# Optimization experiments

Hardware: AMD Instinct MI355X
Metric: run time of the kernel (lower is better)

Reference implementation:

```python
import jax, jax.numpy as jnp
import numpy as np

N_NODE = 100000
EMB = 100
BATCH = 512
SEQ = 50
LAYERS = 2
NNZ = 1000000
BETA = 0.01


def setup_inputs() -> dict:
    key = jax.random.key(0)
    ks = jax.random.split(key, 16)
    stdv = 1.0 / np.sqrt(EMB)
    u = lambda k, shp: jax.random.uniform(k, shp, jnp.float32, -stdv, stdv)
    emb_weight = u(ks[0], (N_NODE, EMB))
    pos_weight = u(ks[1], (200, EMB))
    w_1 = u(ks[2], (2 * EMB, EMB))
    w_2 = u(ks[3], (EMB, 1))
    glu1_w = u(ks[4], (EMB, EMB))
    glu1_b = u(ks[5], (EMB,))
    glu2_w = u(ks[6], (EMB, EMB))
    # sparse hypergraph adjacency in COO form
    adj_rows = jax.random.randint(ks[7], (NNZ,), 0, N_NODE)
    adj_cols = jax.random.randint(ks[8], (NNZ,), 0, N_NODE)
    adj_vals = jax.random.uniform(ks[9], (NNZ,), jnp.float32, 0.0, 0.1)
    session_item = jax.random.randint(ks[10], (BATCH, SEQ), 0, N_NODE + 1)
    reversed_sess_item = jax.random.randint(ks[11], (BATCH, SEQ), 0, N_NODE + 1)
    session_len = jnp.ones((BATCH, 1), jnp.float32)
    mask = jnp.ones((BATCH, SEQ), jnp.float32)
    D = jax.random.uniform(ks[12], (BATCH, BATCH), jnp.float32, 0.0, 0.01)
    A = jax.random.uniform(ks[13], (BATCH, BATCH), jnp.float32, 0.0, 0.01)
    # fixed permutations standing in for torch.randperm in SSL
    perm_rows = jax.random.permutation(ks[14], BATCH)
    perm_cols = jax.random.permutation(ks[15], EMB)
    return {
        'session_item': session_item, 'session_len': session_len, 'D': D, 'A': A,
        'reversed_sess_item': reversed_sess_item, 'mask': mask,
        'emb_weight': emb_weight, 'pos_weight': pos_weight, 'w_1': w_1, 'w_2': w_2,
        'glu1_w': glu1_w, 'glu1_b': glu1_b, 'glu2_w': glu2_w,
        'adj_rows': adj_rows, 'adj_cols': adj_cols, 'adj_vals': adj_vals,
        'perm_rows': perm_rows, 'perm_cols': perm_cols,
    }


def reference(session_item, session_len, D, A, reversed_sess_item, mask,
              emb_weight, pos_weight, w_1, w_2, glu1_w, glu1_b, glu2_w,
              adj_rows, adj_cols, adj_vals, perm_rows, perm_cols):
    # ---- HyperConv: layers of sparse mm, summed over layer outputs ----
    h = emb_weight
    item_hg = h
    for _ in range(LAYERS):
        h = jax.ops.segment_sum(adj_vals[:, None] * h[adj_cols], adj_rows,
                                num_segments=N_NODE)
        item_hg = item_hg + h

    # ---- generate_sess_emb (gather + attention gate) ----
    pad_hg = jnp.concatenate([jnp.zeros((1, EMB), item_hg.dtype), item_hg], 0)
    seq_h = pad_hg[reversed_sess_item]                       # [B, L, d]
    hs = jnp.sum(seq_h, 1) / session_len                     # [B, d]
    pos = jnp.broadcast_to(pos_weight[:SEQ], (BATCH, SEQ, EMB))
    nh = jnp.tanh(jnp.concatenate([pos, seq_h], -1) @ w_1)   # [B, L, d]
    nh = jax.nn.sigmoid(nh @ glu1_w.T + glu1_b + (hs @ glu2_w.T)[:, None, :])
    att = (nh @ w_2) * mask[..., None]                       # [B, L, 1]
    sess_hg = jnp.sum(att * seq_h, 1)                        # [B, d]

    # ---- LineConv (line-graph propagation on raw embedding) ----
    pad0 = jnp.concatenate([jnp.zeros((1, EMB), emb_weight.dtype), emb_weight], 0)
    s = jnp.sum(pad0[session_item], 1) / session_len          # [B, d]
    sess_lg = s
    DA = D @ A
    for _ in range(LAYERS):
        s = DA @ s
        sess_lg = sess_lg + s

    # ---- SSL contrastive loss (fixed permutations replace randperm) ----
    pos_s = jnp.sum(sess_hg * sess_lg, 1)
    corrupt = sess_hg[perm_rows][:, perm_cols]
    neg1 = jnp.sum(sess_lg * corrupt, 1)
    con = jnp.sum(-jnp.log(1e-8 + jax.nn.sigmoid(pos_s))
                  - jnp.log(1e-8 + (1.0 - jax.nn.sigmoid(neg1))))

    # use_HG=True -> sess_emb is the hypergraph session embedding
    return item_hg, sess_hg, BETA * con
```

## Files before the change

### kernel.cpp

```cpp
#include <hip/hip_runtime.h>
#include <math.h>

#define N_NODE 100000
#define EMB    100
#define BATCH  512
#define SEQ    50
#define NNZ    1000000

#define SCAN_CHUNK 1024
#define SCAN_NB ((N_NODE + SCAN_CHUNK - 1) / SCAN_CHUNK)

static __device__ __forceinline__ float bf2f(unsigned short u) {
  union { unsigned int i; float f; } v; v.i = ((unsigned int)u) << 16; return v.f;
}
static __device__ __forceinline__ unsigned short f2bf(float f) {
  union { float f; unsigned int i; } v; v.f = f;
  unsigned int i = v.i;
  return (unsigned short)((i + 0x7fffu + ((i >> 16) & 1u)) >> 16);
}
static __device__ __forceinline__ float lo2f(unsigned int u) {
  union { unsigned int i; float f; } v; v.i = u << 16; return v.f;
}
static __device__ __forceinline__ float hi2f(unsigned int u) {
  union { unsigned int i; float f; } v; v.i = u & 0xffff0000u; return v.f;
}

__global__ void hist_kernel(const int* __restrict__ rows, int* __restrict__ counts) {
  int i = blockIdx.x * blockDim.x + threadIdx.x;
  if (i < NNZ) atomicAdd(&counts[rows[i]], 1);
}

__global__ void scan_partial_kernel(const int* __restrict__ counts, int* __restrict__ partial) {
  __shared__ int red[256];
  int b = blockIdx.x, t = threadIdx.x;
  int base = b * SCAN_CHUNK;
  int s = 0;
  #pragma unroll
  for (int k = 0; k < SCAN_CHUNK; k += 256) {
    int idx = base + k + t;
    if (idx < N_NODE) s += counts[idx];
  }
  red[t] = s;
  __syncthreads();
  for (int off = 128; off; off >>= 1) {
    if (t < off) red[t] += red[t + off];
    __syncthreads();
  }
  if (t == 0) partial[b] = red[0];
}

__global__ void scan_top_kernel(int* __restrict__ partial, int* __restrict__ row_ptr) {
  __shared__ int s[128];
  int t = threadIdx.x;
  int v = (t < SCAN_NB) ? partial[t] : 0;
  s[t] = v;
  __syncthreads();
  for (int off = 1; off < 128; off <<= 1) {
    int u = (t >= off) ? s[t - off] : 0;
    __syncthreads();
    s[t] += u;
    __syncthreads();
  }
  if (t < SCAN_NB) partial[t] = (t == 0) ? 0 : s[t - 1];
  if (t == 127) row_ptr[N_NODE] = s[127];
}

__global__ void scan_final_kernel(const int* __restrict__ partial,
                                  int* __restrict__ counts_cursor,
                                  int* __restrict__ row_ptr) {
  __shared__ int s[256];
  int b = blockIdx.x, t = threadIdx.x;
  int base = b * SCAN_CHUNK + t * 4;
  int c[4];
  #pragma unroll
  for (int k = 0; k < 4; ++k) {
    int idx = base + k;
    c[k] = (idx < N_NODE) ? counts_cursor[idx] : 0;
  }
  int local = c[0] + c[1] + c[2] + c[3];
  s[t] = local;
  __syncthreads();
  for (int off = 1; off < 256; off <<= 1) {
    int u = (t >= off) ? s[t - off] : 0;
    __syncthreads();
    s[t] += u;
    __syncthreads();
  }
  int prefix = partial[b] + ((t == 0) ? 0 : s[t - 1]);
  #pragma unroll
  for (int k = 0; k < 4; ++k) {
    int idx = base + k;
    if (idx < N_NODE) {
      row_ptr[idx] = prefix;
      counts_cursor[idx] = prefix;
      prefix += c[k];
    }
  }
}

__global__ void scatterA_kernel(const int* __restrict__ rows, const int* __restrict__ cols,
                                const float* __restrict__ vals, int* __restrict__ cursor,
                                unsigned int* __restrict__ cv) {
  int i = blockIdx.x * blockDim.x + threadIdx.x;
  if (i >= NNZ) return;
  int p = atomicAdd(&cursor[rows[i]], 1);
  int q = (int)rintf(vals[i] * 327670.f);
  q = q < 0 ? 0 : (q > 32767 ? 32767 : q);
  cv[p] = ((unsigned int)cols[i] << 15) | (unsigned int)q;
}

__global__ void scatterB_kernel(const int* __restrict__ rows, const int* __restrict__ cols,
                                const float* __restrict__ vals, int* __restrict__ cursor,
                                unsigned short* __restrict__ colHi, unsigned char* __restrict__ colLo) {
  int i = blockIdx.x * blockDim.x + threadIdx.x;
  if (i >= NNZ) return;
  int p = atomicAdd(&cursor[rows[i]], 1);
  int c = cols[i];
  int q = (int)rintf(vals[i] * 1270.f);
  q = q < 0 ? 0 : (q > 127 ? 127 : q);
  colHi[p] = (unsigned short)(c >> 1);
  colLo[p] = (unsigned char)(((c & 1) << 7) | q);
}

__global__ void spmmA_kernel(const int* __restrict__ rp, const unsigned int* __restrict__ cv,
                             const float2* __restrict__ gsrc, const float2* __restrict__ base,
                             float2* __restrict__ dst) {
  int w = (blockIdx.x * blockDim.x + threadIdx.x) >> 6;
  int lane = threadIdx.x & 63;
  if (w >= N_NODE || lane >= 50) return;
  int s = __builtin_amdgcn_readfirstlane(rp[w]);
  int e = __builtin_amdgcn_readfirstlane(rp[w + 1]);
  float ax[16], ay[16];
  #pragma unroll
  for (int k = 0; k < 16; ++k) { ax[k] = 0.f; ay[k] = 0.f; }
  for (int j = s; j < e; j += 16) {
    int   cc[16];
    float vv[16];
    #pragma unroll
    for (int k = 0; k < 16; ++k) {
      int jj = j + k;
      int jc = jj < e ? jj : e - 1;
      unsigned int u = cv[jc];
      cc[k] = (int)(u >> 15);
      float v = (float)(u & 0x7fffu) * (1.f / 327670.f);
      vv[k] = (jj < e) ? v : 0.f;
    }
    float2 uu[16];
    #pragma unroll
    for (int k = 0; k < 16; ++k) uu[k] = gsrc[cc[k] * 50 + lane];
    #pragma unroll
    for (int k = 0; k < 16; ++k) { ax[k] += vv[k] * uu[k].x; ay[k] += vv[k] * uu[k].y; }
  }
  #pragma unroll
  for (int k = 0; k < 8; ++k) { ax[k] += ax[k + 8]; ay[k] += ay[k + 8]; }
  #pragma unroll
  for (int k = 0; k < 4; ++k) { ax[k] += ax[k + 4]; ay[k] += ay[k + 4]; }
  float sx = (ax[0] + ax[1]) + (ax[2] + ax[3]);
  float sy = (ay[0] + ay[1]) + (ay[2] + ay[3]);
  float2 ev = base[w * 50 + lane];
  dst[w * 50 + lane] = make_float2(ev.x + sx, ev.y + sy);
}

__global__ void spmmB_kernel(const int* __restrict__ rp, const unsigned short* __restrict__ colHi,
                             const unsigned char* __restrict__ colLo,
                             const float2* __restrict__ gsrc, const float2* __restrict__ base,
                             float2* __restrict__ dst) {
  int w = (blockIdx.x * blockDim.x + threadIdx.x) >> 6;
  int lane = threadIdx.x & 63;
  if (w >= N_NODE || lane >= 50) return;
  int s = __builtin_amdgcn_readfirstlane(rp[w]);
  int e = __builtin_amdgcn_readfirstlane(rp[w + 1]);
  float ax[16], ay[16];
  #pragma unroll
  for (int k = 0; k < 16; ++k) { ax[k] = 0.f; ay[k] = 0.f; }
  for (int j = s; j < e; j += 16) {
    int   cc[16];
    float vv[16];
    #pragma unroll
    for (int k = 0; k < 16; ++k) {
      int jj = j + k;
      int jc = jj < e ? jj : e - 1;
      int hi = colHi[jc], lo = colLo[jc];
      cc[k] = (hi << 1) | (lo >> 7);
      float v = (float)(lo & 0x7f) * (1.f / 1270.f);
      vv[k] = (jj < e) ? v : 0.f;
    }
    float2 uu[16];
    #pragma unroll
    for (int k = 0; k < 16; ++k) uu[k] = gsrc[cc[k] * 50 + lane];
    #pragma unroll
    for (int k = 0; k < 16; ++k) { ax[k] += vv[k] * uu[k].x; ay[k] += vv[k] * uu[k].y; }
  }
  #pragma unroll
  for (int k = 0; k < 8; ++k) { ax[k] += ax[k + 8]; ay[k] += ay[k + 8]; }
  #pragma unroll
  for (int k = 0; k < 4; ++k) { ax[k] += ax[k + 4]; ay[k] += ay[k + 4]; }
  float sx = (ax[0] + ax[1]) + (ax[2] + ax[3]);
  float sy = (ay[0] + ay[1]) + (ay[2] + ay[3]);
  float2 ev = base[w * 50 + lane];
  dst[w * 50 + lane] = make_float2(ev.x + sx, ev.y + sy);
}

__global__ void posw_kernel(const float* __restrict__ pos_w, const float* __restrict__ w1,
                            float* __restrict__ posW) {
  __shared__ float sp[EMB];
  int l = blockIdx.x, e = threadIdx.x;
  if (e < EMB) sp[e] = pos_w[l * EMB + e];
  __syncthreads();
  if (e < EMB) {
    float a = 0.f;
    for (int k = 0; k < EMB; ++k) a += sp[k] * w1[k * EMB + e];
    posW[l * EMB + e] = a;
  }
}

__global__ __launch_bounds__(512, 4) void sess_kernel(
    const int* __restrict__ rsi, const int* __restrict__ si,
    const float* __restrict__ item_hg,
    const float* __restrict__ emb, const float* __restrict__ slen,
    const float* __restrict__ posW, const float* __restrict__ w1,
    const float* __restrict__ glu1w, const float* __restrict__ glu1b,
    const float* __restrict__ glu2w, const float* __restrict__ w2,
    const float* __restrict__ maskp,
    float* __restrict__ X, float* __restrict__ Z,
    float* __restrict__ out_sess) {
  __shared__ __align__(16) float seq[SEQ * EMB];
  __shared__ unsigned int w1p[50 * EMB];
  __shared__ unsigned int g1p[50 * EMB];
  __shared__ float hsL[EMB];
  __shared__ __align__(16) float nhL[4][EMB];
  __shared__ float hsP[4][EMB];
  __shared__ float s0P[4][EMB];
  __shared__ float hsgP[4][EMB];
  __shared__ float accP[4][EMB];
  __shared__ float redg[4][2];
  int b = blockIdx.x, t = threadIdx.x;
  int g = t >> 7;
  int e = t & 127;
  bool act = e < EMB;

  for (int i = t; i < 50 * EMB; i += 512) {
    int kp = i / EMB, e2 = i % EMB;
    unsigned int b0 = f2bf(w1[EMB * EMB + (2 * kp) * EMB + e2]);
    unsigned int b1 = f2bf(w1[EMB * EMB + (2 * kp + 1) * EMB + e2]);
    w1p[i] = b0 | (b1 << 16);
    unsigned int c0 = f2bf(glu1w[e2 * EMB + 2 * kp]);
    unsigned int c1 = f2bf(glu1w[e2 * EMB + 2 * kp + 1]);
    g1p[i] = c0 | (c1 << 16);
  }

  float inv = 1.f / slen[b];

  float hsacc = 0.f, s0acc = 0.f;
  if (act) {
    for (int l = g; l < SEQ; l += 4) {
      int i1 = rsi[b * SEQ + l];
      float sv_ = (i1 > 0) ? item_hg[(i1 - 1) * EMB + e] : 0.f;
      seq[l * EMB + e] = sv_;
      hsacc += sv_;
      int i0 = si[b * SEQ + l];
      if (i0 > 0) s0acc += emb[(i0 - 1) * EMB + e];
    }
    hsP[g][e] = hsacc;
    s0P[g][e] = s0acc;
  }
  __syncthreads();
  if (act && g == 0) {
    float hv = (hsP[0][e] + hsP[1][e] + hsP[2][e] + hsP[3][e]) * inv;
    float sv = (s0P[0][e] + s0P[1][e] + s0P[2][e] + s0P[3][e]) * inv;
    hsL[e] = hv;
    X[b * EMB + e] = sv;
    Z[b * EMB + e] = sv;
  }
  __syncthreads();

  if (act) {
    float a = 0.f;
    int k0 = g * 25;
    for (int k = k0; k < k0 + 25; ++k) a += hsL[k] * glu2w[e * EMB + k];
    hsgP[g][e] = a;
  }
  __syncthreads();
  float hsgv = 0.f, w2v = 0.f;
  if (act) {
    hsgv = glu1b[e] + hsgP[0][e] + hsgP[1][e] + hsgP[2][e] + hsgP[3][e];
    w2v = w2[e];
  }

  float acc = 0.f;
  for (int it = 0; it < (SEQ + 3) / 4; ++it) {
    int l = it * 4 + g;
    bool lv = l < SEQ;
    __syncthreads();
    if (act && lv) {
      const float4* sq4 = (const float4*)&seq[l * EMB];
      float a0 = 0.f, a1 = 0.f, a2 = 0.f, a3 = 0.f;
      #pragma unroll
      for (int i = 0; i < 25; ++i) {
        float4 sv = sq4[i];
        unsigned int p0 = w1p[(2 * i) * EMB + e];
        unsigned int p1 = w1p[(2 * i + 1) * EMB + e];
        a0 += sv.x * lo2f(p0);
        a1 += sv.y * hi2f(p0);
        a2 += sv.z * lo2f(p1);
        a3 += sv.w * hi2f(p1);
      }
      float nh = posW[l * EMB + e] + ((a0 + a1) + (a2 + a3));
      nhL[g][e] = tanhf(nh);
    }
    __syncthreads();
    float p = 0.f;
    if (act && lv) {
      const float4* nq4 = (const float4*)nhL[g];
      float a0 = hsgv, a1 = 0.f, a2 = 0.f, a3 = 0.f;
      #pragma unroll
      for (int i = 0; i < 25; ++i) {
        float4 nv = nq4[i];
        unsigned int p0 = g1p[(2 * i) * EMB + e];
        unsigned int p1 = g1p[(2 * i + 1) * EMB + e];
        a0 += nv.x * lo2f(p0);
        a1 += nv.y * hi2f(p0);
        a2 += nv.z * lo2f(p1);
        a3 += nv.w * hi2f(p1);
      }
      float a = (a0 + a1) + (a2 + a3);
      float gs = 1.f / (1.f + __expf(-a));
      p = gs * w2v;
    }
    for (int off = 32; off; off >>= 1) p += __shfl_down(p, off, 64);
    if ((t & 63) == 0) redg[g][(t >> 6) & 1] = p;
    __syncthreads();
    if (act && lv) {
      float att = (redg[g][0] + redg[g][1]) * maskp[b * SEQ + l];
      acc += att * seq[l * EMB + e];
    }
  }
  if (act) accP[g][e] = acc;
  __syncthreads();
  if (act && g == 0)
    out_sess[b * EMB + e] = accP[0][e] + accP[1][e] + accP[2][e] + accP[3][e];
}

__global__ void mv_kernel(const float* __restrict__ M, const float* __restrict__ x,
                          float* __restrict__ y, float* __restrict__ Zacc) {
  __shared__ float Ms[BATCH];
  int b = blockIdx.x, t = threadIdx.x;
  for (int i = t; i < BATCH; i += 128) Ms[i] = M[b * BATCH + i];
  __syncthreads();
  if (t < EMB) {
    float a = 0.f;
    for (int k = 0; k < BATCH; ++k) a += Ms[k] * x[k * EMB + t];
    y[b * EMB + t] = a;
    if (Zacc) Zacc[b * EMB + t] += a;
  }
}

__global__ void ssl_kernel(const float* __restrict__ Z, const float* __restrict__ hg,
                           const int* __restrict__ pr, const int* __restrict__ pc,
                           float* __restrict__ loss_out) {
  __shared__ float r1[128], r2[128];
  int b = blockIdx.x, t = threadIdx.x;
  float p1 = 0.f, p2 = 0.f;
  if (t < EMB) {
    float lg = Z[b * EMB + t];
    p1 = lg * hg[b * EMB + t];
    p2 = lg * hg[pr[b] * EMB + pc[t]];
  }
  r1[t] = p1; r2[t] = p2;
  __syncthreads();
  for (int off = 64; off; off >>= 1) {
    if (t < off) { r1[t] += r1[t + off]; r2[t] += r2[t + off]; }
    __syncthreads();
  }
  if (t == 0) {
    float sp = 1.f / (1.f + expf(-r1[0]));
    float sn = 1.f / (1.f + expf(-r2[0]));
    atomicAdd(loss_out, 0.01f * (-logf(1e-8f + sp) - logf(1e-8f + (1.f - sn))));
  }
}

extern "C" void kernel_launch(void* const* d_in, const int* in_sizes, int n_in,
                              void* d_out, int out_size, void* d_ws, size_t ws_size,
                              hipStream_t stream) {
  const int*   session_item = (const int*)d_in[0];
  const float* slen   = (const float*)d_in[1];
  const float* D      = (const float*)d_in[2];
  const float* A      = (const float*)d_in[3];
  const int*   rsi    = (const int*)d_in[4];
  const float* mask   = (const float*)d_in[5];
  const float* emb    = (const float*)d_in[6];
  const float* posw   = (const float*)d_in[7];
  const float* w1     = (const float*)d_in[8];
  const float* w2     = (const float*)d_in[9];
  const float* glu1w  = (const float*)d_in[10];
  const float* glu1b  = (const float*)d_in[11];
  const float* glu2w  = (const float*)d_in[12];
  const int*   adj_rows = (const int*)d_in[13];
  const int*   adj_cols = (const int*)d_in[14];
  const float* adj_vals = (const float*)d_in[15];
  const int*   pr     = (const int*)d_in[16];
  const int*   pc     = (const int*)d_in[17];

  float* out_item = (float*)d_out;
  float* out_sess = out_item + (size_t)N_NODE * EMB;
  float* out_loss = out_sess + (size_t)BATCH * EMB;
  float2* out2    = (float2*)d_out;
  const float2* emb2 = (const float2*)emb;

  char* ws = (char*)d_ws;
  size_t off = 0;
  auto alloc = [&](size_t bytes) -> void* {
    void* p = ws + off;
    off = (off + bytes + 255) & ~(size_t)255;
    return p;
  };

  hipMemsetAsync(out_loss, 0, 4, stream);

  if (ws_size >= 5500000) {
    int*          counts  = (int*)alloc((size_t)N_NODE * 4);
    int*          row_ptr = (int*)alloc((size_t)(N_NODE + 1) * 4);
    int*          partial = (int*)alloc((size_t)SCAN_NB * 4);
    unsigned int* cv      = (unsigned int*)alloc((size_t)NNZ * 4);
    float* posW = (float*)alloc((size_t)SEQ * EMB * 4);
    float* X    = (float*)alloc((size_t)BATCH * EMB * 4);
    float* Y    = (float*)alloc((size_t)BATCH * EMB * 4);
    float* Z    = (float*)alloc((size_t)BATCH * EMB * 4);

    hipMemsetAsync(counts, 0, (size_t)N_NODE * 4, stream);

    hist_kernel<<<(NNZ + 255) / 256, 256, 0, stream>>>(adj_rows, counts);
    scan_partial_kernel<<<SCAN_NB, 256, 0, stream>>>(counts, partial);
    scan_top_kernel<<<1, 128, 0, stream>>>(partial, row_ptr);
    scan_final_kernel<<<SCAN_NB, 256, 0, stream>>>(partial, counts, row_ptr);
    scatterA_kernel<<<(NNZ + 255) / 256, 256, 0, stream>>>(adj_rows, adj_cols, adj_vals,
                                                           counts, cv);
    spmmA_kernel<<<N_NODE / 4, 256, 0, stream>>>(row_ptr, cv, emb2, emb2, out2);
    spmmA_kernel<<<N_NODE / 4, 256, 0, stream>>>(row_ptr, cv, out2, emb2, out2);

    posw_kernel<<<SEQ, 128, 0, stream>>>(posw, w1, posW);
    sess_kernel<<<BATCH, 512, 0, stream>>>(rsi, session_item, out_item, emb, slen, posW,
                                           w1, glu1w, glu1b, glu2w, w2, mask,
                                           X, Z, out_sess);
    mv_kernel<<<BATCH, 128, 0, stream>>>(A, X, Y, (float*)nullptr);
    mv_kernel<<<BATCH, 128, 0, stream>>>(D, Y, X, Z);
    mv_kernel<<<BATCH, 128, 0, stream>>>(A, X, Y, (float*)nullptr);
    mv_kernel<<<BATCH, 128, 0, stream>>>(D, Y, X, Z);
    ssl_kernel<<<BATCH, 128, 0, stream>>>(Z, out_sess, pr, pc, out_loss);
  } else {
    unsigned short* colHi  = (unsigned short*)alloc((size_t)NNZ * 2);
    unsigned char*  colLo  = (unsigned char*)alloc((size_t)NNZ);
    int*            row_ptr = (int*)alloc((size_t)(N_NODE + 1) * 4);
    int*            partial = (int*)alloc((size_t)SCAN_NB * 4);
    size_t u0 = off;
    int*   counts = (int*)alloc((size_t)N_NODE * 4);
    off = u0;
    float* posW = (float*)alloc((size_t)SEQ * EMB * 4);
    float* X    = (float*)alloc((size_t)BATCH * EMB * 4);
    float* Y    = (float*)alloc((size_t)BATCH * EMB * 4);
    float* Z    = (float*)alloc((size_t)BATCH * EMB * 4);

    hipMemsetAsync(counts, 0, (size_t)N_NODE * 4, stream);

    hist_kernel<<<(NNZ + 255) / 256, 256, 0, stream>>>(adj_rows, counts);
    scan_partial_kernel<<<SCAN_NB, 256, 0, stream>>>(counts, partial);
    scan_top_kernel<<<1, 128, 0, stream>>>(partial, row_ptr);
    scan_final_kernel<<<SCAN_NB, 256, 0, stream>>>(partial, counts, row_ptr);
    scatterB_kernel<<<(NNZ + 255) / 256, 256, 0, stream>>>(adj_rows, adj_cols, adj_vals,
                                                           counts, colHi, colLo);
    spmmB_kernel<<<N_NODE / 4, 256, 0, stream>>>(row_ptr, colHi, colLo, emb2, emb2, out2);
    spmmB_kernel<<<N_NODE / 4, 256, 0, stream>>>(row_ptr, colHi, colLo, out2, emb2, out2);

    posw_kernel<<<SEQ, 128, 0, stream>>>(posw, w1, posW);
    sess_kernel<<<BATCH, 512, 0, stream>>>(rsi, session_item, out_item, emb, slen, posW,
                                           w1, glu1w, glu1b, glu2w, w2, mask,
                                           X, Z, out_sess);
    mv_kernel<<<BATCH, 128, 0, stream>>>(A, X, Y, (float*)nullptr);
    mv_kernel<<<BATCH, 128, 0, stream>>>(D, Y, X, Z);
    mv_kernel<<<BATCH, 128, 0, stream>>>(A, X, Y, (float*)nullptr);
    mv_kernel<<<BATCH, 128, 0, stream>>>(D, Y, X, Z);
    ssl_kernel<<<BATCH, 128, 0, stream>>>(Z, out_sess, pr, pc, out_loss);
  }
}
```

Measured before the change: 564.8 us.

## Gather bf16-packed embeddings in SpMM, pre-pack weights, fuse small kernels

Before the SpMMs, the embedding table is converted to a bf16-packed copy, optionally padded to a 64-word row stride, so each gathered neighbour row reads half as many bytes. The first layer writes its result as bf16 for the second layer to gather. The histogram, embedding pack, weight pack and pos-weight matmul are merged into one launch. sess_kernel now copies pre-packed weights instead of converting them in every block, and the last mv is fused with the SSL loss. This cuts gather bandwidth and launch count, but adds a pass over the table, needs more workspace, and reduces precision of the intermediate layer output.

```diff
diff --git a/kernel.cpp b/kernel.cpp
--- a/kernel.cpp
+++ b/kernel.cpp
@@ -9,6 +9,9 @@
 
 #define SCAN_CHUNK 1024
 #define SCAN_NB ((N_NODE + SCAN_CHUNK - 1) / SCAN_CHUNK)
+#define HIST_NB ((NNZ + 255) / 256)
+#define PACKW_NB 20
+#define POSW_NB  SEQ
 
 static __device__ __forceinline__ float bf2f(unsigned short u) {
   union { unsigned int i; float f; } v; v.i = ((unsigned int)u) << 16; return v.f;
@@ -24,10 +27,67 @@
 static __device__ __forceinline__ float hi2f(unsigned int u) {
   union { unsigned int i; float f; } v; v.i = u & 0xffff0000u; return v.f;
 }
+static __device__ __forceinline__ unsigned int packbf2(float x, float y) {
+  return (unsigned int)f2bf(x) | ((unsigned int)f2bf(y) << 16);
+}
 
 __global__ void hist_kernel(const int* __restrict__ rows, int* __restrict__ counts) {
   int i = blockIdx.x * blockDim.x + threadIdx.x;
   if (i < NNZ) atomicAdd(&counts[rows[i]], 1);
+}
+
+__global__ void fused_pre_kernel(const int* __restrict__ rows, int* __restrict__ counts,
+                                 const float2* __restrict__ src, unsigned int* __restrict__ ebf,
+                                 int stride, int packBlocks,
+                                 const float* __restrict__ w1, const float* __restrict__ glu1w,
+                                 unsigned int* __restrict__ w1pG, unsigned int* __restrict__ g1pG,
+                                 const float* __restrict__ pos_w, float* __restrict__ posW) {
+  __shared__ float sp[EMB];
+  int blk = blockIdx.x, t = threadIdx.x;
+  if (blk < HIST_NB) {
+    int i = blk * 256 + t;
+    if (i < NNZ) atomicAdd(&counts[rows[i]], 1);
+  } else if (blk < HIST_NB + packBlocks) {
+    int i = (blk - HIST_NB) * 256 + t;
+    if (i < N_NODE * stride) {
+      int w, c;
+      if (stride == 64) { w = i >> 6; c = i & 63; }
+      else              { w = i / 50; c = i - w * 50; }
+      unsigned int out = 0u;
+      if (c < 50) {
+        float2 v = src[w * 50 + c];
+        out = packbf2(v.x, v.y);
+      }
+      ebf[i] = out;
+    }
+  } else if (blk < HIST_NB + packBlocks + PACKW_NB) {
+    int i = (blk - HIST_NB - packBlocks) * 256 + t;
+    if (i < 50 * EMB) {
+      int kp = i / EMB, e = i % EMB;
+      w1pG[i] = packbf2(w1[EMB * EMB + (2 * kp) * EMB + e],
+                        w1[EMB * EMB + (2 * kp + 1) * EMB + e]);
+      g1pG[i] = packbf2(glu1w[e * EMB + 2 * kp], glu1w[e * EMB + 2 * kp + 1]);
+    }
+  } else {
+    int l = blk - HIST_NB - packBlocks - PACKW_NB;
+    if (t < EMB) sp[t] = pos_w[l * EMB + t];
+    __syncthreads();
+    if (t < EMB) {
+      float a = 0.f;
+      for (int k = 0; k < EMB; ++k) a += sp[k] * w1[k * EMB + t];
+      posW[l * EMB + t] = a;
+    }
+  }
+}
+
+__global__ void packw_kernel(const float* __restrict__ w1, const float* __restrict__ glu1w,
+                             unsigned int* __restrict__ w1pG, unsigned int* __restrict__ g1pG) {
+  int i = blockIdx.x * blockDim.x + threadIdx.x;
+  if (i >= 50 * EMB) return;
+  int kp = i / EMB, e = i % EMB;
+  w1pG[i] = packbf2(w1[EMB * EMB + (2 * kp) * EMB + e],
+                    w1[EMB * EMB + (2 * kp + 1) * EMB + e]);
+  g1pG[i] = packbf2(glu1w[e * EMB + 2 * kp], glu1w[e * EMB + 2 * kp + 1]);
 }
 
 __global__ void scan_partial_kernel(const int* __restrict__ counts, int* __restrict__ partial) {
@@ -122,9 +182,9 @@
   colLo[p] = (unsigned char)(((c & 1) << 7) | q);
 }
 
-__global__ void spmmA_kernel(const int* __restrict__ rp, const unsigned int* __restrict__ cv,
-                             const float2* __restrict__ gsrc, const float2* __restrict__ base,
-                             float2* __restrict__ dst) {
+template<int STRIDE>
+__global__ void spmmP1_kernel(const int* __restrict__ rp, const unsigned int* __restrict__ cv,
+                              const float2* __restrict__ emb2, unsigned int* __restrict__ ebf) {
   int w = (blockIdx.x * blockDim.x + threadIdx.x) >> 6;
   int lane = threadIdx.x & 63;
   if (w >= N_NODE || lane >= 50) return;
@@ -145,11 +205,11 @@
       float v = (float)(u & 0x7fffu) * (1.f / 327670.f);
       vv[k] = (jj < e) ? v : 0.f;
     }
-    float2 uu[16];
-    #pragma unroll
-    for (int k = 0; k < 16; ++k) uu[k] = gsrc[cc[k] * 50 + lane];
-    #pragma unroll
-    for (int k = 0; k < 16; ++k) { ax[k] += vv[k] * uu[k].x; ay[k] += vv[k] * uu[k].y; }
+    unsigned int uu[16];
+    #pragma unroll
+    for (int k = 0; k < 16; ++k) uu[k] = ebf[cc[k] * STRIDE + lane];
+    #pragma unroll
+    for (int k = 0; k < 16; ++k) { ax[k] += vv[k] * lo2f(uu[k]); ay[k] += vv[k] * hi2f(uu[k]); }
   }
   #pragma unroll
   for (int k = 0; k < 8; ++k) { ax[k] += ax[k + 8]; ay[k] += ay[k + 8]; }
@@ -157,7 +217,47 @@
   for (int k = 0; k < 4; ++k) { ax[k] += ax[k + 4]; ay[k] += ay[k + 4]; }
   float sx = (ax[0] + ax[1]) + (ax[2] + ax[3]);
   float sy = (ay[0] + ay[1]) + (ay[2] + ay[3]);
-  float2 ev = base[w * 50 + lane];
+  float2 ev = emb2[w * 50 + lane];
+  ebf[w * STRIDE + lane] = packbf2(ev.x + sx, ev.y + sy);
+}
+
+template<int STRIDE>
+__global__ void spmmP2_kernel(const int* __restrict__ rp, const unsigned int* __restrict__ cv,
+                              const unsigned int* __restrict__ ebf,
+                              const float2* __restrict__ emb2, float2* __restrict__ dst) {
+  int w = (blockIdx.x * blockDim.x + threadIdx.x) >> 6;
+  int lane = threadIdx.x & 63;
+  if (w >= N_NODE || lane >= 50) return;
+  int s = __builtin_amdgcn_readfirstlane(rp[w]);
+  int e = __builtin_amdgcn_readfirstlane(rp[w + 1]);
+  float ax[16], ay[16];
+  #pragma unroll
+  for (int k = 0; k < 16; ++k) { ax[k] = 0.f; ay[k] = 0.f; }
+  for (int j = s; j < e; j += 16) {
+    int   cc[16];
+    float vv[16];
+    #pragma unroll
+    for (int k = 0; k < 16; ++k) {
+      int jj = j + k;
+      int jc = jj < e ? jj : e - 1;
+      unsigned int u = cv[jc];
+      cc[k] = (int)(u >> 15);
+      float v = (float)(u & 0x7fffu) * (1.f / 327670.f);
+      vv[k] = (jj < e) ? v : 0.f;
+    }
+    unsigned int uu[16];
+    #pragma unroll
+    for (int k = 0; k < 16; ++k) uu[k] = ebf[cc[k] * STRIDE + lane];
+    #pragma unroll
+    for (int k = 0; k < 16; ++k) { ax[k] += vv[k] * lo2f(uu[k]); ay[k] += vv[k] * hi2f(uu[k]); }
+  }
+  #pragma unroll
+  for (int k = 0; k < 8; ++k) { ax[k] += ax[k + 8]; ay[k] += ay[k + 8]; }
+  #pragma unroll
+  for (int k = 0; k < 4; ++k) { ax[k] += ax[k + 4]; ay[k] += ay[k + 4]; }
+  float sx = (ax[0] + ax[1]) + (ax[2] + ax[3]);
+  float sy = (ay[0] + ay[1]) + (ay[2] + ay[3]);
+  float2 ev = emb2[w * 50 + lane];
   dst[w * 50 + lane] = make_float2(ev.x + sx, ev.y + sy);
 }
 
@@ -218,15 +318,16 @@
     const int* __restrict__ rsi, const int* __restrict__ si,
     const float* __restrict__ item_hg,
     const float* __restrict__ emb, const float* __restrict__ slen,
-    const float* __restrict__ posW, const float* __restrict__ w1,
-    const float* __restrict__ glu1w, const float* __restrict__ glu1b,
+    const float* __restrict__ posW,
+    const unsigned int* __restrict__ w1pG, const unsigned int* __restrict__ g1pG,
+    const float* __restrict__ glu1b,
     const float* __restrict__ glu2w, const float* __restrict__ w2,
     const float* __restrict__ maskp,
     float* __restrict__ X, float* __restrict__ Z,
     float* __restrict__ out_sess) {
   __shared__ __align__(16) float seq[SEQ * EMB];
-  __shared__ unsigned int w1p[50 * EMB];
-  __shared__ unsigned int g1p[50 * EMB];
+  __shared__ __align__(16) unsigned int w1p[50 * EMB];
+  __shared__ __align__(16) unsigned int g1p[50 * EMB];
   __shared__ float hsL[EMB];
   __shared__ __align__(16) float nhL[4][EMB];
   __shared__ float hsP[4][EMB];
@@ -239,14 +340,12 @@
   int e = t & 127;
   bool act = e < EMB;
 
-  for (int i = t; i < 50 * EMB; i += 512) {
-    int kp = i / EMB, e2 = i % EMB;
-    unsigned int b0 = f2bf(w1[EMB * EMB + (2 * kp) * EMB + e2]);
-    unsigned int b1 = f2bf(w1[EMB * EMB + (2 * kp + 1) * EMB + e2]);
-    w1p[i] = b0 | (b1 << 16);
-    unsigned int c0 = f2bf(glu1w[e2 * EMB + 2 * kp]);
-    unsigned int c1 = f2bf(glu1w[e2 * EMB + 2 * kp + 1]);
-    g1p[i] = c0 | (c1 << 16);
+  {
+    const uint4* s1 = (const uint4*)w1pG;
+    const uint4* s2 = (const uint4*)g1pG;
+    uint4* d1 = (uint4*)w1p;
+    uint4* d2 = (uint4*)g1p;
+    for (int i = t; i < 1250; i += 512) { d1[i] = s1[i]; d2[i] = s2[i]; }
   }
 
   float inv = 1.f / slen[b];
@@ -355,16 +454,22 @@
   }
 }
 
-__global__ void ssl_kernel(const float* __restrict__ Z, const float* __restrict__ hg,
-                           const int* __restrict__ pr, const int* __restrict__ pc,
-                           float* __restrict__ loss_out) {
+__global__ void mv_ssl_kernel(const float* __restrict__ D, const float* __restrict__ Y,
+                              const float* __restrict__ Zprev, const float* __restrict__ hg,
+                              const int* __restrict__ pr, const int* __restrict__ pc,
+                              float* __restrict__ loss_out) {
+  __shared__ float Ms[BATCH];
   __shared__ float r1[128], r2[128];
   int b = blockIdx.x, t = threadIdx.x;
+  for (int i = t; i < BATCH; i += 128) Ms[i] = D[b * BATCH + i];
+  __syncthreads();
   float p1 = 0.f, p2 = 0.f;
   if (t < EMB) {
-    float lg = Z[b * EMB + t];
-    p1 = lg * hg[b * EMB + t];
-    p2 = lg * hg[pr[b] * EMB + pc[t]];
+    float a = 0.f;
+    for (int k = 0; k < BATCH; ++k) a += Ms[k] * Y[k * EMB + t];
+    float z = Zprev[b * EMB + t] + a;
+    p1 = z * hg[b * EMB + t];
+    p2 = z * hg[pr[b] * EMB + pc[t]];
   }
   r1[t] = p1; r2[t] = p2;
   __syncthreads();
@@ -417,36 +522,48 @@
 
   hipMemsetAsync(out_loss, 0, 4, stream);
 
-  if (ws_size >= 5500000) {
+  if (ws_size >= 31500000 || (ws_size >= 25500000)) {
+    bool wide = ws_size >= 31500000;
+    int stride = wide ? 64 : 50;
+    int packBlocks = (N_NODE * stride + 255) / 256;
+
     int*          counts  = (int*)alloc((size_t)N_NODE * 4);
     int*          row_ptr = (int*)alloc((size_t)(N_NODE + 1) * 4);
     int*          partial = (int*)alloc((size_t)SCAN_NB * 4);
     unsigned int* cv      = (unsigned int*)alloc((size_t)NNZ * 4);
+    unsigned int* ebf     = (unsigned int*)alloc((size_t)N_NODE * stride * 4);
     float* posW = (float*)alloc((size_t)SEQ * EMB * 4);
     float* X    = (float*)alloc((size_t)BATCH * EMB * 4);
     float* Y    = (float*)alloc((size_t)BATCH * EMB * 4);
     float* Z    = (float*)alloc((size_t)BATCH * EMB * 4);
+    unsigned int* w1pG = (unsigned int*)alloc((size_t)50 * EMB * 4);
+    unsigned int* g1pG = (unsigned int*)alloc((size_t)50 * EMB * 4);
 
     hipMemsetAsync(counts, 0, (size_t)N_NODE * 4, stream);
 
-    hist_kernel<<<(NNZ + 255) / 256, 256, 0, stream>>>(adj_rows, counts);
+    fused_pre_kernel<<<HIST_NB + packBlocks + PACKW_NB + POSW_NB, 256, 0, stream>>>(
+        adj_rows, counts, emb2, ebf, stride, packBlocks,
+        w1, glu1w, w1pG, g1pG, posw, posW);
     scan_partial_kernel<<<SCAN_NB, 256, 0, stream>>>(counts, partial);
     scan_top_kernel<<<1, 128, 0, stream>>>(partial, row_ptr);
     scan_final_kernel<<<SCAN_NB, 256, 0, stream>>>(partial, counts, row_ptr);
     scatterA_kernel<<<(NNZ + 255) / 256, 256, 0, stream>>>(adj_rows, adj_cols, adj_vals,
                                                            counts, cv);
-    spmmA_kernel<<<N_NODE / 4, 256, 0, stream>>>(row_ptr, cv, emb2, emb2, out2);
-    spmmA_kernel<<<N_NODE / 4, 256, 0, stream>>>(row_ptr, cv, out2, emb2, out2);
-
-    posw_kernel<<<SEQ, 128, 0, stream>>>(posw, w1, posW);
+    if (wide) {
+      spmmP1_kernel<64><<<N_NODE / 4, 256, 0, stream>>>(row_ptr, cv, emb2, ebf);
+      spmmP2_kernel<64><<<N_NODE / 4, 256, 0, stream>>>(row_ptr, cv, ebf, emb2, out2);
+    } else {
+      spmmP1_kernel<50><<<N_NODE / 4, 256, 0, stream>>>(row_ptr, cv, emb2, ebf);
+      spmmP2_kernel<50><<<N_NODE / 4, 256, 0, stream>>>(row_ptr, cv, ebf, emb2, out2);
+    }
+
     sess_kernel<<<BATCH, 512, 0, stream>>>(rsi, session_item, out_item, emb, slen, posW,
-                                           w1, glu1w, glu1b, glu2w, w2, mask,
+                                           w1pG, g1pG, glu1b, glu2w, w2, mask,
                                            X, Z, out_sess);
     mv_kernel<<<BATCH, 128, 0, stream>>>(A, X, Y, (float*)nullptr);
     mv_kernel<<<BATCH, 128, 0, stream>>>(D, Y, X, Z);
     mv_kernel<<<BATCH, 128, 0, stream>>>(A, X, Y, (float*)nullptr);
-    mv_kernel<<<BATCH, 128, 0, stream>>>(D, Y, X, Z);
-    ssl_kernel<<<BATCH, 128, 0, stream>>>(Z, out_sess, pr, pc, out_loss);
+    mv_ssl_kernel<<<BATCH, 128, 0, stream>>>(D, Y, Z, out_sess, pr, pc, out_loss);
   } else {
     unsigned short* colHi  = (unsigned short*)alloc((size_t)NNZ * 2);
     unsigned char*  colLo  = (unsigned char*)alloc((size_t)NNZ);
@@ -459,10 +576,12 @@
     float* X    = (float*)alloc((size_t)BATCH * EMB * 4);
     float* Y    = (float*)alloc((size_t)BATCH * EMB * 4);
     float* Z    = (float*)alloc((size_t)BATCH * EMB * 4);
+    unsigned int* w1pG = (unsigned int*)alloc((size_t)50 * EMB * 4);
+    unsigned int* g1pG = (unsigned int*)alloc((size_t)50 * EMB * 4);
 
     hipMemsetAsync(counts, 0, (size_t)N_NODE * 4, stream);
 
-    hist_kernel<<<(NNZ + 255) / 256, 256, 0, stream>>>(adj_rows, counts);
+    hist_kernel<<<HIST_NB, 256, 0, stream>>>(adj_rows, counts);
     scan_partial_kernel<<<SCAN_NB, 256, 0, stream>>>(counts, partial);
     scan_top_kernel<<<1, 128, 0, stream>>>(partial, row_ptr);
     scan_final_kernel<<<SCAN_NB, 256, 0, stream>>>(partial, counts, row_ptr);
@@ -471,14 +590,14 @@
     spmmB_kernel<<<N_NODE / 4, 256, 0, stream>>>(row_ptr, colHi, colLo, emb2, emb2, out2);
     spmmB_kernel<<<N_NODE / 4, 256, 0, stream>>>(row_ptr, colHi, colLo, out2, emb2, out2);
 
+    packw_kernel<<<PACKW_NB, 256, 0, stream>>>(w1, glu1w, w1pG, g1pG);
     posw_kernel<<<SEQ, 128, 0, stream>>>(posw, w1, posW);
     sess_kernel<<<BATCH, 512, 0, stream>>>(rsi, session_item, out_item, emb, slen, posW,
-                                           w1, glu1w, glu1b, glu2w, w2, mask,
+                                           w1pG, g1pG, glu1b, glu2w, w2, mask,
                                            X, Z, out_sess);
     mv_kernel<<<BATCH, 128, 0, stream>>>(A, X, Y, (float*)nullptr);
     mv_kernel<<<BATCH, 128, 0, stream>>>(D, Y, X, Z);
     mv_kernel<<<BATCH, 128, 0, stream>>>(A, X, Y, (float*)nullptr);
-    mv_kernel<<<BATCH, 128, 0, stream>>>(D, Y, X, Z);
-    ssl_kernel<<<BATCH, 128, 0, stream>>>(Z, out_sess, pr, pc, out_loss);
-  }
-}
+    mv_ssl_kernel<<<BATCH, 128, 0, stream>>>(D, Y, Z, out_sess, pr, pc, out_loss);
+  }
+}
```

After: 524.1 us. 7.2% less time.
